# Kernel optimization log

Hardware: AMD Instinct MI355X
Metric: run time of the kernel (lower is better)

## Reference

```python
import jax, jax.numpy as jnp
import numpy as np

B, H, W, C = 32, 56, 56, 128
WS, NH, DEPTH = 7, 4, 2
SHIFT = WS // 2
N = WS * WS
HID = 4 * C
CPB = 512


def _layernorm(x, g, b, eps=1e-5):
    m = x.mean(-1, keepdims=True)
    v = ((x - m) ** 2).mean(-1, keepdims=True)
    return (x - m) * jax.lax.rsqrt(v + eps) * g + b


def _window_partition(x):
    b, h, w, c = x.shape
    x = x.reshape(b, h // WS, WS, w // WS, WS, c)
    return x.transpose(0, 1, 3, 2, 4, 5).reshape(-1, N, c)


def _window_reverse(xw, h, w):
    c = xw.shape[-1]
    b = xw.shape[0] // ((h // WS) * (w // WS))
    x = xw.reshape(b, h // WS, w // WS, WS, WS, c)
    return x.transpose(0, 1, 3, 2, 4, 5).reshape(b, h, w, c)


def _rel_index():
    coords = np.stack(np.meshgrid(np.arange(WS), np.arange(WS), indexing='ij'))
    flat = coords.reshape(2, -1)
    rel = (flat[:, :, None] - flat[:, None, :]).transpose(1, 2, 0).astype(np.int64)
    rel[..., 0] += WS - 1
    rel[..., 1] += WS - 1
    rel[..., 0] *= 2 * WS - 1
    return jnp.asarray(rel.sum(-1))  # [N, N]


def _coords_table():
    # SwinV2 log-spaced continuous relative coords table (pretrained_window_size=0 path)
    r = np.arange(-(WS - 1), WS, dtype=np.float32)
    t = np.stack(np.meshgrid(r, r, indexing='ij'), axis=-1)  # [2W-1, 2W-1, 2]
    t = t / (WS - 1) * 8.0
    t = np.sign(t) * np.log2(np.abs(t) + 1.0) / np.log2(8.0)
    return jnp.asarray(t.reshape(-1, 2))  # [(2W-1)^2, 2]


def _shift_mask():
    img = np.zeros((H, W), np.float32)
    cnt = 0
    for hs in (slice(0, -WS), slice(-WS, -SHIFT), slice(-SHIFT, None)):
        for ws_ in (slice(0, -WS), slice(-WS, -SHIFT), slice(-SHIFT, None)):
            img[hs, ws_] = cnt
            cnt += 1
    mw = np.asarray(_window_partition(jnp.asarray(img)[None, :, :, None])).reshape(-1, N)
    diff = mw[:, None, :] - mw[:, :, None]
    return jnp.asarray(np.where(diff != 0, -100.0, 0.0).astype(np.float32))  # [nW, N, N]


def _forward(x, qkv_w, q_bias, v_bias, logit_scale, cpb_w1, cpb_b1, cpb_w2,
             proj_w, proj_b, norm1_g, norm1_b, mlp_w1, mlp_b1, mlp_w2, mlp_b2,
             norm2_g, norm2_b, pm_g, pm_b, pm_w):
    rel_idx = _rel_index()
    table = _coords_table()
    smask = _shift_mask()
    for i in range(DEPTH):
        shift = 0 if i % 2 == 0 else SHIFT
        xs = jnp.roll(x, (-shift, -shift), axis=(1, 2)) if shift else x
        xw = _window_partition(xs)  # [B*nW, N, C]
        bias = jnp.concatenate([q_bias[i], jnp.zeros_like(q_bias[i]), v_bias[i]])
        qkv = (xw @ qkv_w[i] + bias).reshape(-1, N, 3, NH, C // NH).transpose(2, 0, 3, 1, 4)
        q, k, v = qkv[0], qkv[1], qkv[2]  # [B*nW, NH, N, hd]
        qn = q / jnp.maximum(jnp.linalg.norm(q, axis=-1, keepdims=True), 1e-12)
        kn = k / jnp.maximum(jnp.linalg.norm(k, axis=-1, keepdims=True), 1e-12)
        scale = jnp.exp(jnp.minimum(logit_scale[i], jnp.log(100.0)))  # [NH,1,1]
        attn = jnp.einsum('bhnd,bhmd->bhnm', qn, kn) * scale
        rpb = 16.0 * jax.nn.sigmoid(
            (jax.nn.relu(table @ cpb_w1[i] + cpb_b1[i]) @ cpb_w2[i])[rel_idx])  # [N,N,NH]
        attn = attn + rpb.transpose(2, 0, 1)[None]
        if shift:
            nW = smask.shape[0]
            attn = (attn.reshape(-1, nW, NH, N, N) + smask[None, :, None]).reshape(-1, NH, N, N)
        attn = jax.nn.softmax(attn, axis=-1)
        out = jnp.einsum('bhnm,bhmd->bnhd', attn, v).reshape(-1, N, C)
        out = out @ proj_w[i] + proj_b[i]
        xs = _window_reverse(out, H, W)
        if shift:
            xs = jnp.roll(xs, (shift, shift), axis=(1, 2))
        # SwinV2 post-norm residuals
        x = x + _layernorm(xs, norm1_g[i], norm1_b[i])
        y = jax.nn.gelu(x @ mlp_w1[i] + mlp_b1[i], approximate=False) @ mlp_w2[i] + mlp_b2[i]
        x = x + _layernorm(y, norm2_g[i], norm2_b[i])
    # PatchMerging: [B,H,W,C] -> [B,H/2,W/2,4C] -> norm -> Linear(4C,2C)
    xm = x.reshape(B, H // 2, 2, W // 2, 2, C).transpose(0, 1, 3, 2, 4, 5)
    xm = xm.reshape(B, H // 2, W // 2, 4 * C)
    return _layernorm(xm, pm_g, pm_b) @ pm_w


def setup_inputs() -> dict:
    key = jax.random.key(0)
    ks = jax.random.split(key, 8)
    s = 0.02
    rn = lambda k, shp: jax.random.normal(k, shp, jnp.float32) * s
    return dict(
        x=jax.random.normal(ks[0], (B, H, W, C), jnp.float32),
        qkv_w=rn(ks[1], (DEPTH, C, 3 * C)),
        q_bias=jnp.zeros((DEPTH, C), jnp.float32),
        v_bias=jnp.zeros((DEPTH, C), jnp.float32),
        logit_scale=jnp.full((DEPTH, NH, 1, 1), np.log(10.0), jnp.float32),
        cpb_w1=rn(ks[2], (DEPTH, 2, CPB)),
        cpb_b1=jnp.zeros((DEPTH, CPB), jnp.float32),
        cpb_w2=rn(ks[3], (DEPTH, CPB, NH)),
        proj_w=rn(ks[4], (DEPTH, C, C)),
        proj_b=jnp.zeros((DEPTH, C), jnp.float32),
        norm1_g=jnp.ones((DEPTH, C), jnp.float32),
        norm1_b=jnp.zeros((DEPTH, C), jnp.float32),
        mlp_w1=rn(ks[5], (DEPTH, C, HID)),
        mlp_b1=jnp.zeros((DEPTH, HID), jnp.float32),
        mlp_w2=rn(ks[6], (DEPTH, HID, C)),
        mlp_b2=jnp.zeros((DEPTH, C), jnp.float32),
        norm2_g=jnp.ones((DEPTH, C), jnp.float32),
        norm2_b=jnp.zeros((DEPTH, C), jnp.float32),
        pm_g=jnp.ones((4 * C,), jnp.float32),
        pm_b=jnp.zeros((4 * C,), jnp.float32),
        pm_w=rn(ks[7], (4 * C, 2 * C)),
    )


def reference(x, qkv_w, q_bias, v_bias, logit_scale, cpb_w1, cpb_b1, cpb_w2,
              proj_w, proj_b, norm1_g, norm1_b, mlp_w1, mlp_b1, mlp_w2, mlp_b2,
              norm2_g, norm2_b, pm_g, pm_b, pm_w):
    return _forward(x, qkv_w, q_bias, v_bias, logit_scale, cpb_w1, cpb_b1, cpb_w2,
                    proj_w, proj_b, norm1_g, norm1_b, mlp_w1, mlp_b1, mlp_w2, mlp_b2,
                    norm2_g, norm2_b, pm_g, pm_b, pm_w)
```

## Files before the change

### kernel.cpp

```cpp
#include <hip/hip_runtime.h>
#include <math.h>


namespace {
constexpr int kTok = 32 * 56 * 56;
}

typedef __attribute__((ext_vector_type(8))) short bf16x8;
typedef __attribute__((ext_vector_type(4))) float f32x4;

union FragU {
    int4 i4;
    bf16x8 b8;
    unsigned short u[8];
};

__device__ __forceinline__ short f2bf(float f) {
    unsigned u = __float_as_uint(f);
    return (short)((u + 0x7FFFu + ((u >> 16) & 1u)) >> 16);
}
__device__ __forceinline__ float bf2f(unsigned short u) {
    return __uint_as_float(((unsigned)u) << 16);
}
__device__ __forceinline__ unsigned cvt_pk_bf16(float a, float b) {
    unsigned r;
    asm("v_cvt_pk_bf16_f32 %0, %1, %2" : "=v"(r) : "v"(a), "v"(b));
    return r;
}
__device__ __forceinline__ float gelu_t(float x) {
    float x2 = x * x;
    float t0 = fmaf(0.044715f * x2, x, x);
    float e = exp2f(2.3022227f * t0);
    float r = __builtin_amdgcn_rcpf(e + 1.0f);
    return fmaf(-x, r, x);
}

__global__ __launch_bounds__(256) void k_cpb(
    const float* __restrict__ w1, const float* __restrict__ b1,
    const float* __restrict__ w2, float* __restrict__ out169) {
    int L = blockIdx.x / 169;
    int t = blockIdx.x % 169;
    const float* w1L = w1 + L * 1024;
    const float* b1L = b1 + L * 512;
    const float* w2L = w2 + L * 2048;
    float* outL = out169 + L * 704;
    int ia = t / 13, ib = t % 13;
    float r0 = (float)(ia - 6) * (8.0f / 6.0f);
    float s0 = (r0 > 0.f) ? 1.f : (r0 < 0.f ? -1.f : 0.f);
    float t0 = s0 * log2f(fabsf(r0) + 1.0f) * (1.0f / 3.0f);
    float r1 = (float)(ib - 6) * (8.0f / 6.0f);
    float s1 = (r1 > 0.f) ? 1.f : (r1 < 0.f ? -1.f : 0.f);
    float t1 = s1 * log2f(fabsf(r1) + 1.0f) * (1.0f / 3.0f);

    int tid = threadIdx.x;
    float p0 = 0, p1 = 0, p2 = 0, p3 = 0;
    for (int c = tid; c < 512; c += 256) {
        float hv = fmaxf(t0 * w1L[c] + t1 * w1L[512 + c] + b1L[c], 0.0f);
        p0 += hv * w2L[c * 4 + 0];
        p1 += hv * w2L[c * 4 + 1];
        p2 += hv * w2L[c * 4 + 2];
        p3 += hv * w2L[c * 4 + 3];
    }
    __shared__ float red[256][4];
    red[tid][0] = p0; red[tid][1] = p1; red[tid][2] = p2; red[tid][3] = p3;
    __syncthreads();
    for (int s = 128; s > 0; s >>= 1) {
        if (tid < s) {
            red[tid][0] += red[tid + s][0];
            red[tid][1] += red[tid + s][1];
            red[tid][2] += red[tid + s][2];
            red[tid][3] += red[tid + s][3];
        }
        __syncthreads();
    }
    if (tid < 4) outL[t * 4 + tid] = red[0][tid];
}

__global__ void k_rpb(const float* __restrict__ out169, float* __restrict__ rpb64) {
    int e2 = blockIdx.x * 256 + threadIdx.x;
    int L = e2 >> 14, e = e2 & 16383;
    int h = e >> 12, r = e & 4095;
    int i = r >> 6, j = r & 63;
    float val;
    if (j >= 49) {
        val = -30000.0f;
    } else if (i >= 49) {
        val = 0.0f;
    } else {
        int dp = i / 7 - j / 7 + 6;
        int dq = i % 7 - j % 7 + 6;
        float v = out169[L * 704 + (dp * 13 + dq) * 4 + h];
        val = 16.0f / (1.0f + expf(-v));
    }
    rpb64[e2] = val;
}

__device__ __forceinline__ void cvt_slot(
    const float* __restrict__ W, short* __restrict__ Wb, int slt, int Kb, int N) {
    int nn = slt & 63;
    int tmp = slt >> 6;
    int kb = tmp % Kb;
    int nt = tmp / Kb;
    int n = nt * 64 + nn;
    int k0 = kb * 8;
    union { int4 i4; short s8[8]; } u;
#pragma unroll
    for (int e = 0; e < 8; ++e) u.s8[e] = f2bf(W[(size_t)(k0 + e) * N + n]);
    int nns = (nn & ~3) | ((nn ^ kb) & 3);
    *(int4*)(Wb + (((size_t)tmp) * 64 + nns) * 8) = u.i4;
}

__global__ __launch_bounds__(256) void k_cvtall(
    const float* __restrict__ qkv_w, const float* __restrict__ proj_w,
    const float* __restrict__ mw1, const float* __restrict__ mw2,
    const float* __restrict__ pmw, short* __restrict__ wall) {
    int s = blockIdx.x * 256 + threadIdx.x;
    short* wqkvb  = wall;
    short* wprojb = wall + 98304;
    short* wm1b   = wall + 131072;
    short* wm2b   = wall + 262144;
    short* wpmb   = wall + 393216;
    if (s < 12288) {
        int L = s / 6144, r = s % 6144;
        cvt_slot(qkv_w + L * 49152, wqkvb + L * 49152, r, 16, 384);
    } else if (s < 16384) {
        int s2 = s - 12288;
        int L = s2 / 2048, r = s2 % 2048;
        cvt_slot(proj_w + L * 16384, wprojb + L * 16384, r, 16, 128);
    } else if (s < 32768) {
        int s2 = s - 16384;
        int L = s2 / 8192, r = s2 % 8192;
        cvt_slot(mw1 + L * 65536, wm1b + L * 65536, r, 16, 512);
    } else if (s < 49152) {
        int s2 = s - 32768;
        int L = s2 / 8192, r = s2 % 8192;
        cvt_slot(mw2 + L * 65536, wm2b + L * 65536, r, 64, 128);
    } else {
        cvt_slot(pmw, wpmb, s - 49152, 64, 256);
    }
}

__global__ __launch_bounds__(256) void k_cvtx(
    const float* __restrict__ x, short* __restrict__ xb) {
    size_t e = ((size_t)blockIdx.x * 256 + threadIdx.x) * 8;
    const float* src = x + e;
    float4 f0 = *(const float4*)src;
    float4 f1 = *(const float4*)(src + 4);
    union { int4 i4; short s8[8]; } u;
    u.s8[0] = f2bf(f0.x); u.s8[1] = f2bf(f0.y);
    u.s8[2] = f2bf(f0.z); u.s8[3] = f2bf(f0.w);
    u.s8[4] = f2bf(f1.x); u.s8[5] = f2bf(f1.y);
    u.s8[6] = f2bf(f1.z); u.s8[7] = f2bf(f1.w);
    *(int4*)(xb + e) = u.i4;
}

template <int K, int EPI, int NT>
__global__ __launch_bounds__(256) void k_gemm(
    const short* __restrict__ Ain, const short* __restrict__ Wb,
    const float* __restrict__ bias0, const float* __restrict__ bias1,
    void* __restrict__ Out, int ostride, int shift) {
    constexpr int Kb = K / 8;
    constexpr int NC = K / 128;
    __shared__ int4 As4[2048];
    __shared__ int4 Ws4[1024];
    int tid = threadIdx.x;
    int nwg = gridDim.x;
    int chunk = nwg >> 3;
    int lid = (blockIdx.x & 7) * chunk + (blockIdx.x >> 3);
    int mt = lid / NT, nt = lid - mt * NT;
    int mb = mt * 128;
    int w = tid >> 6, l = tid & 63, lr = l & 15, lg = l >> 4;
    const f32x4 fz = {0.f, 0.f, 0.f, 0.f};
    f32x4 acc[2][4];
#pragma unroll
    for (int mi = 0; mi < 2; ++mi)
#pragma unroll
        for (int ni = 0; ni < 4; ++ni) acc[mi][ni] = fz;

    for (int c = 0; c < NC; ++c) {
        if (c) __syncthreads();
#pragma unroll
        for (int it = 0; it < 8; ++it) {
            int s = it * 256 + tid;
            int m = s >> 4, kb = s & 15;
            int gm = mb + m;
            if (EPI == 1 && shift) {
                int b = gm / 3136, r = gm % 3136;
                int hh = r / 56 + shift; if (hh >= 56) hh -= 56;
                int ww = r % 56 + shift; if (ww >= 56) ww -= 56;
                gm = b * 3136 + hh * 56 + ww;
            }
            int slot = kb * 128 + ((m & ~7) | ((m ^ kb) & 7));
            As4[slot] = *(const int4*)(Ain + (size_t)gm * K + c * 128 + kb * 8);
        }
        {
            const int4* wsrc = (const int4*)(Wb + ((size_t)nt * Kb + c * 16) * 64 * 8);
#pragma unroll
            for (int it = 0; it < 4; ++it) Ws4[it * 256 + tid] = wsrc[it * 256 + tid];
        }
        __syncthreads();
#pragma unroll
        for (int kk = 0; kk < 4; ++kk) {
            int kbl = kk * 4 + lg;
            int m0 = w * 32 + lr;
            bf16x8 a0 = *(const bf16x8*)&As4[kbl * 128 + ((m0 & ~7) | ((m0 ^ kbl) & 7))];
            int m1 = m0 + 16;
            bf16x8 a1 = *(const bf16x8*)&As4[kbl * 128 + ((m1 & ~7) | ((m1 ^ kbl) & 7))];
#pragma unroll
            for (int ni = 0; ni < 4; ++ni) {
                int nn = lr + 16 * ni;
                bf16x8 bfr = *(const bf16x8*)&Ws4[kbl * 64 + ((nn & ~3) | ((nn ^ kbl) & 3))];
                acc[0][ni] = __builtin_amdgcn_mfma_f32_16x16x32_bf16(a0, bfr, acc[0][ni], 0, 0, 0);
                acc[1][ni] = __builtin_amdgcn_mfma_f32_16x16x32_bf16(a1, bfr, acc[1][ni], 0, 0, 0);
            }
        }
    }
#pragma unroll
    for (int ni = 0; ni < 4; ++ni) {
        int col = nt * 64 + ni * 16 + lr;
        float bv = 0.f;
        if (EPI == 1) bv = (col < 128) ? bias0[col] : ((col < 256) ? 0.f : bias1[col - 256]);
#pragma unroll
        for (int mi = 0; mi < 2; ++mi) {
#pragma unroll
            for (int r = 0; r < 4; ++r) {
                int row = mb + w * 32 + mi * 16 + lg * 4 + r;
                float v = acc[mi][ni][r] + bv;
                if (EPI == 0) {
                    ((float*)Out)[(size_t)row * ostride + col] = v;
                } else {
                    ((short*)Out)[(size_t)row * 384 + col] = f2bf(v);
                }
            }
        }
    }
}

template <int K, bool RF32>
__global__ __launch_bounds__(256) void k_gemm_ln(
    const short* __restrict__ Ain, const short* __restrict__ Wb,
    const float* __restrict__ bias, const float* __restrict__ g,
    const float* __restrict__ bt, const void* __restrict__ resid,
    short* __restrict__ xoutb, int shift) {
    constexpr int Kb = K / 8;
    constexpr int NC = K / 128;
    __shared__ int4 As4[1024];
    __shared__ int4 Ws4[2048];
    int tid = threadIdx.x;
    int mb = blockIdx.x * 64;
    int w = tid >> 6, l = tid & 63, lr = l & 15, lg = l >> 4;
    const f32x4 fz = {0.f, 0.f, 0.f, 0.f};
    f32x4 acc[8];
#pragma unroll
    for (int ni = 0; ni < 8; ++ni) acc[ni] = fz;

    for (int c = 0; c < NC; ++c) {
        if (c) __syncthreads();
#pragma unroll
        for (int it = 0; it < 4; ++it) {
            int s = it * 256 + tid;
            int m = s >> 4, kb = s & 15;
            int slot = kb * 64 + ((m & ~7) | ((m ^ kb) & 7));
            As4[slot] = *(const int4*)(Ain + (size_t)(mb + m) * K + c * 128 + kb * 8);
        }
        {
            const int4* w0 = (const int4*)(Wb + ((size_t)(c * 16)) * 64 * 8);
            const int4* w1 = (const int4*)(Wb + ((size_t)(Kb + c * 16)) * 64 * 8);
#pragma unroll
            for (int it = 0; it < 4; ++it) {
                Ws4[it * 256 + tid] = w0[it * 256 + tid];
                Ws4[1024 + it * 256 + tid] = w1[it * 256 + tid];
            }
        }
        __syncthreads();
#pragma unroll
        for (int kk = 0; kk < 4; ++kk) {
            int kbl = kk * 4 + lg;
            int m0 = w * 16 + lr;
            bf16x8 a0 = *(const bf16x8*)&As4[kbl * 64 + ((m0 & ~7) | ((m0 ^ kbl) & 7))];
#pragma unroll
            for (int ni = 0; ni < 8; ++ni) {
                int nn = lr + 16 * (ni & 3);
                bf16x8 bfr = *(const bf16x8*)&Ws4[(ni >> 2) * 1024 + kbl * 64 +
                                                  ((nn & ~3) | ((nn ^ kbl) & 3))];
                acc[ni] = __builtin_amdgcn_mfma_f32_16x16x32_bf16(a0, bfr, acc[ni], 0, 0, 0);
            }
        }
    }
    float bv[8], gv[8], btv[8];
#pragma unroll
    for (int ni = 0; ni < 8; ++ni) {
        int col = ni * 16 + lr;
        bv[ni] = bias[col]; gv[ni] = g[col]; btv[ni] = bt[col];
    }
#pragma unroll
    for (int r = 0; r < 4; ++r) {
        int row = mb + w * 16 + lg * 4 + r;
        float v[8];
        float s1 = 0.f, s2 = 0.f;
#pragma unroll
        for (int ni = 0; ni < 8; ++ni) {
            v[ni] = acc[ni][r] + bv[ni];
            s1 += v[ni];
            s2 = fmaf(v[ni], v[ni], s2);
        }
#pragma unroll
        for (int off = 8; off >= 1; off >>= 1) {
            s1 += __shfl_xor(s1, off);
            s2 += __shfl_xor(s2, off);
        }
        float mean = s1 * (1.0f / 128.0f);
        float var = s2 * (1.0f / 128.0f) - mean * mean;
        float rstd = rsqrtf(var + 1e-5f);
        int mo = row;
        if (shift) {
            int b = row / 3136, rr = row % 3136;
            int hh = rr / 56 + shift; if (hh >= 56) hh -= 56;
            int ww = rr % 56 + shift; if (ww >= 56) ww -= 56;
            mo = b * 3136 + hh * 56 + ww;
        }
        size_t base = (size_t)mo * 128;
#pragma unroll
        for (int ni = 0; ni < 8; ++ni) {
            int col = ni * 16 + lr;
            float rv = RF32 ? ((const float*)resid)[base + col]
                            : bf2f(((const unsigned short*)resid)[base + col]);
            float o = rv + (v[ni] - mean) * rstd * gv[ni] + btv[ni];
            xoutb[base + col] = f2bf(o);
        }
    }
}

__global__ __launch_bounds__(256) void k_mlp(
    short* __restrict__ xb, const short* __restrict__ W1b,
    const short* __restrict__ W2b, const float* __restrict__ b1,
    const float* __restrict__ b2, const float* __restrict__ g,
    const float* __restrict__ bt) {
    __shared__ int4 W1s[1024];
    __shared__ int4 W2s[1024];
    __shared__ short Hs[4 * 2304];
    int tid = threadIdx.x;
    int mb = blockIdx.x * 128;
    int w = tid >> 6, l = tid & 63, lr = l & 15, lg = l >> 4;
    const f32x4 fz = {0.f, 0.f, 0.f, 0.f};
    short* Hw = Hs + w * 2304;

    int4 xfrag[2][4];
#pragma unroll
    for (int mi = 0; mi < 2; ++mi)
#pragma unroll
        for (int kk = 0; kk < 4; ++kk)
            xfrag[mi][kk] = *(const int4*)(
                xb + (size_t)(mb + w * 32 + mi * 16 + lr) * 128 + kk * 32 + lg * 8);

    f32x4 acc2[2][8];
#pragma unroll
    for (int mi = 0; mi < 2; ++mi)
#pragma unroll
        for (int ni = 0; ni < 8; ++ni) acc2[mi][ni] = fz;

    int4 wr0, wr1, wr2, wr3, wr4, wr5, wr6, wr7;
#define LOADW(c)                                                            \
    {                                                                       \
        const int4* w1src = (const int4*)(W1b + (size_t)(c) * 8192);        \
        wr0 = w1src[tid]; wr1 = w1src[256 + tid];                           \
        wr2 = w1src[512 + tid]; wr3 = w1src[768 + tid];                     \
        const int4* w2a = (const int4*)(W2b + (size_t)((c) * 8) * 512);     \
        const int4* w2c = (const int4*)(W2b + (size_t)(64 + (c) * 8) * 512);\
        wr4 = w2a[tid]; wr5 = w2a[256 + tid];                               \
        wr6 = w2c[tid]; wr7 = w2c[256 + tid];                               \
    }
#define STOREW()                                                            \
    {                                                                       \
        W1s[tid] = wr0; W1s[256 + tid] = wr1;                               \
        W1s[512 + tid] = wr2; W1s[768 + tid] = wr3;                         \
        W2s[tid] = wr4; W2s[256 + tid] = wr5;                               \
        W2s[512 + tid] = wr6; W2s[768 + tid] = wr7;                         \
    }

    LOADW(0);
    STOREW();
    __syncthreads();

    for (int c = 0; c < 8; ++c) {
        if (c < 7) LOADW(c + 1);
        f32x4 a1[2][4];
#pragma unroll
        for (int mi = 0; mi < 2; ++mi)
#pragma unroll
            for (int ct = 0; ct < 4; ++ct) a1[mi][ct] = fz;
        __builtin_amdgcn_s_setprio(1);
#pragma unroll
        for (int kk = 0; kk < 4; ++kk) {
            int kbl = kk * 4 + lg;
            FragU xa0; xa0.i4 = xfrag[0][kk];
            FragU xa1; xa1.i4 = xfrag[1][kk];
#pragma unroll
            for (int ct = 0; ct < 4; ++ct) {
                int nn = lr + 16 * ct;
                bf16x8 w1f = *(const bf16x8*)&W1s[kbl * 64 + ((nn & ~3) | ((nn ^ kbl) & 3))];
                a1[0][ct] = __builtin_amdgcn_mfma_f32_16x16x32_bf16(w1f, xa0.b8, a1[0][ct], 0, 0, 0);
                a1[1][ct] = __builtin_amdgcn_mfma_f32_16x16x32_bf16(w1f, xa1.b8, a1[1][ct], 0, 0, 0);
            }
        }
        __builtin_amdgcn_s_setprio(0);
#pragma unroll
        for (int mi = 0; mi < 2; ++mi) {
#pragma unroll
            for (int ct = 0; ct < 4; ++ct) {
                float4 bb = *(const float4*)(b1 + c * 64 + ct * 16 + lg * 4);
                float h0 = gelu_t(a1[mi][ct][0] + bb.x);
                float h1 = gelu_t(a1[mi][ct][1] + bb.y);
                float h2 = gelu_t(a1[mi][ct][2] + bb.z);
                float h3 = gelu_t(a1[mi][ct][3] + bb.w);
                unsigned p0 = cvt_pk_bf16(h0, h1);
                unsigned p1 = cvt_pk_bf16(h2, h3);
                *(int2*)&Hw[(mi * 16 + lr) * 72 + ct * 16 + lg * 4] =
                    make_int2((int)p0, (int)p1);
            }
        }
        __builtin_amdgcn_s_setprio(1);
#pragma unroll
        for (int kc = 0; kc < 2; ++kc) {
            int kbl = kc * 4 + lg;
            FragU ha0; ha0.i4 = *(const int4*)&Hw[lr * 72 + kc * 32 + lg * 8];
            FragU ha1; ha1.i4 = *(const int4*)&Hw[(16 + lr) * 72 + kc * 32 + lg * 8];
#pragma unroll
            for (int ni = 0; ni < 8; ++ni) {
                int nn = lr + 16 * (ni & 3);
                bf16x8 w2f = *(const bf16x8*)&W2s[(ni >> 2) * 512 + kbl * 64 +
                                                  ((nn & ~3) | ((nn ^ kbl) & 3))];
                acc2[0][ni] = __builtin_amdgcn_mfma_f32_16x16x32_bf16(ha0.b8, w2f, acc2[0][ni], 0, 0, 0);
                acc2[1][ni] = __builtin_amdgcn_mfma_f32_16x16x32_bf16(ha1.b8, w2f, acc2[1][ni], 0, 0, 0);
            }
        }
        __builtin_amdgcn_s_setprio(0);
        if (c < 7) {
            __syncthreads();
            STOREW();
            __syncthreads();
        }
    }
#undef LOADW
#undef STOREW

    float bv[8], gv[8], btv[8];
#pragma unroll
    for (int ni = 0; ni < 8; ++ni) {
        int col = ni * 16 + lr;
        bv[ni] = b2[col]; gv[ni] = g[col]; btv[ni] = bt[col];
    }
#pragma unroll
    for (int mi = 0; mi < 2; ++mi) {
#pragma unroll
        for (int r = 0; r < 4; ++r) {
            int row = mb + w * 32 + mi * 16 + lg * 4 + r;
            float v[8];
            float s1 = 0.f, s2 = 0.f;
#pragma unroll
            for (int ni = 0; ni < 8; ++ni) {
                v[ni] = acc2[mi][ni][r] + bv[ni];
                s1 += v[ni];
                s2 = fmaf(v[ni], v[ni], s2);
            }
#pragma unroll
            for (int off = 8; off >= 1; off >>= 1) {
                s1 += __shfl_xor(s1, off);
                s2 += __shfl_xor(s2, off);
            }
            float mean = s1 * (1.0f / 128.0f);
            float var = s2 * (1.0f / 128.0f) - mean * mean;
            float rstd = rsqrtf(var + 1e-5f);
            size_t base = (size_t)row * 128;
#pragma unroll
            for (int ni = 0; ni < 8; ++ni) {
                int col = ni * 16 + lr;
                float rv = bf2f(((const unsigned short*)xb)[base + col]);
                float o = rv + (v[ni] - mean) * rstd * gv[ni] + btv[ni];
                xb[base + col] = f2bf(o);
            }
        }
    }
}

__global__ __launch_bounds__(256) void k_attn(
    const short* __restrict__ qkv, const float* __restrict__ rpb64,
    const float* __restrict__ ls, short* __restrict__ aout, int shift) {
    __shared__ short lds[4 * 3584];
    int wid = blockIdx.x;
    int b = wid >> 6, wrem = wid & 63;
    int wh = wrem >> 3, ww_ = wrem & 7;
    int h = threadIdx.x >> 6;
    int l = threadIdx.x & 63, lr = l & 15, lg = l >> 4;
    short* Pt = lds + h * 3584;
    short* Vt = Pt + 1152;
    float* invks = (float*)(Vt + 2304);
    int tokbase = b * 3136 + wh * 7 * 56 + ww_ * 7;

    float scale = __expf(fminf(ls[h], 4.6051702f));
    int4 qf[4], kf[4], vf[4];
    const int4 zero4 = make_int4(0, 0, 0, 0);
#pragma unroll
    for (int t = 0; t < 4; ++t) {
        int i = t * 16 + lr;
        bool valid = (i < 49);
        int tok = tokbase + (i / 7) * 56 + (i % 7);
        const short* base = qkv + (size_t)tok * 384 + h * 32 + lg * 8;
        qf[t] = valid ? *(const int4*)base : zero4;
        kf[t] = valid ? *(const int4*)(base + 128) : zero4;
    }
#pragma unroll
    for (int t = 0; t < 4; ++t) {
        int e = t * 64 + l;
        int j = e >> 2, dq = e & 3;
        if (j < 49) {
            int tok = tokbase + (j / 7) * 56 + (j % 7);
            vf[t] = *(const int4*)(qkv + (size_t)tok * 384 + 256 + h * 32 + dq * 8);
        } else {
            vf[t] = zero4;
        }
    }

    float invq[4];
#pragma unroll
    for (int t = 0; t < 4; ++t) {
        {
            FragU u; u.i4 = qf[t];
            float ss = 0.f;
#pragma unroll
            for (int e = 0; e < 8; ++e) { float x = bf2f(u.u[e]); ss = fmaf(x, x, ss); }
            ss += __shfl_xor(ss, 16);
            ss += __shfl_xor(ss, 32);
            invq[t] = scale / fmaxf(sqrtf(ss), 1e-12f);
        }
        {
            FragU u; u.i4 = kf[t];
            float ss = 0.f;
#pragma unroll
            for (int e = 0; e < 8; ++e) { float x = bf2f(u.u[e]); ss = fmaf(x, x, ss); }
            ss += __shfl_xor(ss, 16);
            ss += __shfl_xor(ss, 32);
            float ik = 1.0f / fmaxf(sqrtf(ss), 1e-12f);
            if (l < 16) invks[t * 16 + l] = ik;
        }
    }

    for (int t = l; t < 480; t += 64) {
        Vt[(t / 15) * 72 + 49 + (t % 15)] = 0;
    }
#pragma unroll
    for (int t = 0; t < 4; ++t) {
        int e = t * 64 + l;
        int j = e >> 2, dq = e & 3;
        if (j < 49) {
            FragU u; u.i4 = vf[t];
#pragma unroll
            for (int ee = 0; ee < 8; ++ee) Vt[(dq * 8 + ee) * 72 + j] = (short)u.u[ee];
        }
    }

    float ika[4][4];
#pragma unroll
    for (int jt = 0; jt < 4; ++jt) {
        float4 v4 = *(const float4*)&invks[jt * 16 + lg * 4];
        ika[jt][0] = v4.x; ika[jt][1] = v4.y; ika[jt][2] = v4.z; ika[jt][3] = v4.w;
    }

    bool edge = (shift != 0) && ((wh == 7) || (ww_ == 7));
    const float* rbase = rpb64 + h * 4096;
    const f32x4 fz = {0.f, 0.f, 0.f, 0.f};
    f32x4 oacc[2][4];
#pragma unroll
    for (int mi = 0; mi < 2; ++mi)
#pragma unroll
        for (int ni = 0; ni < 4; ++ni) oacc[mi][ni] = fz;

#pragma unroll
    for (int qt = 0; qt < 4; ++qt) {
        f32x4 at[4];
        __builtin_amdgcn_s_setprio(1);
#pragma unroll
        for (int jt = 0; jt < 4; ++jt) {
            FragU a; a.i4 = kf[jt];
            FragU bq; bq.i4 = qf[qt];
            at[jt] = __builtin_amdgcn_mfma_f32_16x16x32_bf16(a.b8, bq.b8, fz, 0, 0, 0);
        }
        __builtin_amdgcn_s_setprio(0);

        float iq = invq[qt];
        int qi = qt * 16 + lr;
        int qc = (qi < 49) ? qi : 48;
        int rlq = 0, clq = 0;
        if (edge) {
            rlq = (wh == 7) ? ((qc / 7) < 4 ? 1 : 2) : 0;
            clq = (ww_ == 7) ? ((qc % 7) < 4 ? 1 : 2) : 0;
        }
#pragma unroll
        for (int jt = 0; jt < 4; ++jt) {
            float4 rv = *(const float4*)(rbase + qc * 64 + jt * 16 + lg * 4);
            float rr[4] = {rv.x, rv.y, rv.z, rv.w};
#pragma unroll
            for (int r = 0; r < 4; ++r) {
                float v = fmaf(at[jt][r] * ika[jt][r], iq, rr[r]);
                if (edge) {
                    int j = jt * 16 + lg * 4 + r;
                    int jc = (j < 49) ? j : 48;
                    int rlk = (wh == 7) ? ((jc / 7) < 4 ? 1 : 2) : 0;
                    int clk = (ww_ == 7) ? ((jc % 7) < 4 ? 1 : 2) : 0;
                    if (rlk != rlq || clk != clq) v -= 100.0f;
                }
                at[jt][r] = v;
            }
        }
        float m = -1e30f;
#pragma unroll
        for (int jt = 0; jt < 4; ++jt)
#pragma unroll
            for (int r = 0; r < 4; ++r) m = fmaxf(m, at[jt][r]);
        m = fmaxf(m, __shfl_xor(m, 16));
        m = fmaxf(m, __shfl_xor(m, 32));
        float s = 0.f;
#pragma unroll
        for (int jt = 0; jt < 4; ++jt)
#pragma unroll
            for (int r = 0; r < 4; ++r) {
                float p = __expf(at[jt][r] - m);
                at[jt][r] = p;
                s += p;
            }
        s += __shfl_xor(s, 16);
        s += __shfl_xor(s, 32);
        float inv = 1.0f / s;
#pragma unroll
        for (int jt = 0; jt < 4; ++jt) {
            unsigned lo = cvt_pk_bf16(at[jt][0] * inv, at[jt][1] * inv);
            unsigned hi = cvt_pk_bf16(at[jt][2] * inv, at[jt][3] * inv);
            *(int2*)&Pt[lr * 72 + jt * 16 + lg * 4] = make_int2((int)lo, (int)hi);
        }
        __builtin_amdgcn_s_setprio(1);
#pragma unroll
        for (int kc = 0; kc < 2; ++kc) {
            FragU pb;
            pb.i4 = *(const int4*)&Pt[lr * 72 + kc * 32 + lg * 8];
#pragma unroll
            for (int mi = 0; mi < 2; ++mi) {
                FragU va;
                va.i4 = *(const int4*)&Vt[(mi * 16 + lr) * 72 + kc * 32 + lg * 8];
                oacc[mi][qt] = __builtin_amdgcn_mfma_f32_16x16x32_bf16(
                    va.b8, pb.b8, oacc[mi][qt], 0, 0, 0);
            }
        }
        __builtin_amdgcn_s_setprio(0);
    }

#pragma unroll
    for (int ni = 0; ni < 4; ++ni) {
        int qrow = ni * 16 + lr;
        if (qrow < 49) {
            int tok = tokbase + (qrow / 7) * 56 + (qrow % 7);
#pragma unroll
            for (int mi = 0; mi < 2; ++mi) {
                unsigned lo = cvt_pk_bf16(oacc[mi][ni][0], oacc[mi][ni][1]);
                unsigned hi = cvt_pk_bf16(oacc[mi][ni][2], oacc[mi][ni][3]);
                *(int2*)&aout[(size_t)tok * 128 + h * 32 + mi * 16 + lg * 4] =
                    make_int2((int)lo, (int)hi);
            }
        }
    }
}

__global__ __launch_bounds__(256) void k_pmln(
    const short* __restrict__ x, const float* __restrict__ g,
    const float* __restrict__ bt, short* __restrict__ outb) {
    int m2 = blockIdx.x * 4 + (threadIdx.x >> 6);
    int l = threadIdx.x & 63;
    int b = m2 / 784, r = m2 % 784;
    int h2 = r / 28, w2 = r % 28;
    int q0 = l * 8;
    int i2 = q0 >> 8, j2 = (q0 >> 7) & 1, c = q0 & 127;
    const short* src = x + (size_t)((b * 56 + 2 * h2 + i2) * 56 + 2 * w2 + j2) * 128 + c;
    FragU u; u.i4 = *(const int4*)src;
    float v[8];
#pragma unroll
    for (int e = 0; e < 8; ++e) v[e] = bf2f(u.u[e]);
    float s1 = 0.f, s2 = 0.f;
#pragma unroll
    for (int e = 0; e < 8; ++e) { s1 += v[e]; s2 = fmaf(v[e], v[e], s2); }
#pragma unroll
    for (int off = 32; off >= 1; off >>= 1) {
        s1 += __shfl_xor(s1, off);
        s2 += __shfl_xor(s2, off);
    }
    float mean = s1 * (1.0f / 512.0f);
    float var = s2 * (1.0f / 512.0f) - mean * mean;
    float rstd = rsqrtf(var + 1e-5f);
    union { int4 i4; short s8[8]; } o;
#pragma unroll
    for (int e = 0; e < 8; ++e)
        o.s8[e] = f2bf((v[e] - mean) * rstd * g[q0 + e] + bt[q0 + e]);
    *(int4*)(outb + (size_t)m2 * 512 + q0) = o.i4;
}

extern "C" void kernel_launch(void* const* d_in, const int* in_sizes, int n_in,
                              void* d_out, int out_size, void* d_ws, size_t ws_size,
                              hipStream_t stream) {
    const float* x_in   = (const float*)d_in[0];
    const float* qkv_w  = (const float*)d_in[1];
    const float* q_bias = (const float*)d_in[2];
    const float* v_bias = (const float*)d_in[3];
    const float* lscale = (const float*)d_in[4];
    const float* cpb_w1 = (const float*)d_in[5];
    const float* cpb_b1 = (const float*)d_in[6];
    const float* cpb_w2 = (const float*)d_in[7];
    const float* proj_w = (const float*)d_in[8];
    const float* proj_b = (const float*)d_in[9];
    const float* n1g    = (const float*)d_in[10];
    const float* n1b    = (const float*)d_in[11];
    const float* mw1    = (const float*)d_in[12];
    const float* mb1    = (const float*)d_in[13];
    const float* mw2    = (const float*)d_in[14];
    const float* mb2    = (const float*)d_in[15];
    const float* n2g    = (const float*)d_in[16];
    const float* n2b    = (const float*)d_in[17];
    const float* pmg    = (const float*)d_in[18];
    const float* pmb    = (const float*)d_in[19];
    const float* pmw    = (const float*)d_in[20];
    float* out = (float*)d_out;

    float* wsf    = (float*)d_ws;
    short* wall   = (short*)wsf;
    short* wqkvb  = wall;
    short* wprojb = wall + 98304;
    short* wm1b   = wall + 131072;
    short* wm2b   = wall + 262144;
    short* wpmb   = wall + 393216;
    float* out169 = wsf + 262144;
    float* rpb64  = out169 + 1408;

    float* R1      = wsf + (size_t)12845056;
    short* qkvb    = (short*)R1;
    short* attnout = (short*)(R1 + (size_t)19267584);
    short* pmin    = (short*)R1;
    short* xb      = (short*)(R1 + (size_t)25690112);

    k_cvtall<<<256, 256, 0, stream>>>(qkv_w, proj_w, mw1, mw2, pmw, wall);
    k_cpb<<<338, 256, 0, stream>>>(cpb_w1, cpb_b1, cpb_w2, out169);
    k_rpb<<<128, 256, 0, stream>>>(out169, rpb64);
    k_cvtx<<<6272, 256, 0, stream>>>(x_in, xb);

    for (int i = 0; i < 2; ++i) {
        int shift = i ? 3 : 0;
        k_gemm<128, 1, 6><<<4704, 256, 0, stream>>>(
            xb, wqkvb + i * 49152, q_bias + i * 128, v_bias + i * 128,
            qkvb, 384, shift);
        k_attn<<<2048, 256, 0, stream>>>(
            qkvb, rpb64 + i * 16384, lscale + i * 4, attnout, shift);
        if (i == 0) {
            k_gemm_ln<128, true><<<1568, 256, 0, stream>>>(
                attnout, wprojb, proj_b, n1g, n1b, x_in, xb, shift);
        } else {
            k_gemm_ln<128, false><<<1568, 256, 0, stream>>>(
                attnout, wprojb + 16384, proj_b + 128, n1g + 128, n1b + 128,
                xb, xb, shift);
        }
        k_mlp<<<784, 256, 0, stream>>>(
            xb, wm1b + i * 65536, wm2b + i * 65536, mb1 + i * 512,
            mb2 + i * 128, n2g + i * 128, n2b + i * 128);
    }
    k_pmln<<<6272, 256, 0, stream>>>(xb, pmg, pmb, pmin);
    k_gemm<512, 0, 4><<<784, 256, 0, stream>>>(
        pmin, wpmb, nullptr, nullptr, out, 256, 0);
}
```

Before: 380.4 us.

## Fuse QKV projection into window attention kernel and drop MLP weight prefetch

The separate QKV GEMM kernel is removed. Each attention workgroup now computes its window's 49x384 QKV tile with MFMA straight from the bf16 activations, handling the shift, and stages it in LDS. This avoids writing and re-reading the full QKV tensor through global memory and removes one launch per layer, at the cost of more LDS per block and each block re-reading the QKV weights. The MLP kernel's register-prefetch double buffering of weights is also replaced by plain synchronous loads into LDS, which may expose load latency.

Result: faster. 354.8 us (-6.7%).

```diff
diff --git a/kernel.cpp b/kernel.cpp
--- a/kernel.cpp
+++ b/kernel.cpp
@@ -113,7 +113,9 @@
 __global__ __launch_bounds__(256) void k_cvtall(
     const float* __restrict__ qkv_w, const float* __restrict__ proj_w,
     const float* __restrict__ mw1, const float* __restrict__ mw2,
-    const float* __restrict__ pmw, short* __restrict__ wall) {
+    const float* __restrict__ pmw, const float* __restrict__ qb,
+    const float* __restrict__ vb, short* __restrict__ wall,
+    float* __restrict__ bias384) {
     int s = blockIdx.x * 256 + threadIdx.x;
     short* wqkvb  = wall;
     short* wprojb = wall + 98304;
@@ -135,8 +137,14 @@
         int s2 = s - 32768;
         int L = s2 / 8192, r = s2 % 8192;
         cvt_slot(mw2 + L * 65536, wm2b + L * 65536, r, 64, 128);
-    } else {
+    } else if (s < 65536) {
         cvt_slot(pmw, wpmb, s - 49152, 64, 256);
+    } else if (s < 66304) {
+        int t = s - 65536;
+        int L = t / 384, f = t % 384;
+        float v = (f < 128) ? qb[L * 128 + f]
+                            : ((f < 256) ? 0.0f : vb[L * 128 + f - 256]);
+        bias384[t] = v;
     }
 }
 
@@ -154,11 +162,10 @@
     *(int4*)(xb + e) = u.i4;
 }
 
-template <int K, int EPI, int NT>
+template <int K, int NT>
 __global__ __launch_bounds__(256) void k_gemm(
     const short* __restrict__ Ain, const short* __restrict__ Wb,
-    const float* __restrict__ bias0, const float* __restrict__ bias1,
-    void* __restrict__ Out, int ostride, int shift) {
+    float* __restrict__ Out, int ostride) {
     constexpr int Kb = K / 8;
     constexpr int NC = K / 128;
     __shared__ int4 As4[2048];
@@ -183,15 +190,8 @@
         for (int it = 0; it < 8; ++it) {
             int s = it * 256 + tid;
             int m = s >> 4, kb = s & 15;
-            int gm = mb + m;
-            if (EPI == 1 && shift) {
-                int b = gm / 3136, r = gm % 3136;
-                int hh = r / 56 + shift; if (hh >= 56) hh -= 56;
-                int ww = r % 56 + shift; if (ww >= 56) ww -= 56;
-                gm = b * 3136 + hh * 56 + ww;
-            }
             int slot = kb * 128 + ((m & ~7) | ((m ^ kb) & 7));
-            As4[slot] = *(const int4*)(Ain + (size_t)gm * K + c * 128 + kb * 8);
+            As4[slot] = *(const int4*)(Ain + (size_t)(mb + m) * K + c * 128 + kb * 8);
         }
         {
             const int4* wsrc = (const int4*)(Wb + ((size_t)nt * Kb + c * 16) * 64 * 8);
@@ -218,19 +218,12 @@
 #pragma unroll
     for (int ni = 0; ni < 4; ++ni) {
         int col = nt * 64 + ni * 16 + lr;
-        float bv = 0.f;
-        if (EPI == 1) bv = (col < 128) ? bias0[col] : ((col < 256) ? 0.f : bias1[col - 256]);
 #pragma unroll
         for (int mi = 0; mi < 2; ++mi) {
 #pragma unroll
             for (int r = 0; r < 4; ++r) {
                 int row = mb + w * 32 + mi * 16 + lg * 4 + r;
-                float v = acc[mi][ni][r] + bv;
-                if (EPI == 0) {
-                    ((float*)Out)[(size_t)row * ostride + col] = v;
-                } else {
-                    ((short*)Out)[(size_t)row * 384 + col] = f2bf(v);
-                }
+                Out[(size_t)row * ostride + col] = acc[mi][ni][r];
             }
         }
     }
@@ -359,31 +352,21 @@
 #pragma unroll
         for (int ni = 0; ni < 8; ++ni) acc2[mi][ni] = fz;
 
-    int4 wr0, wr1, wr2, wr3, wr4, wr5, wr6, wr7;
-#define LOADW(c)                                                            \
-    {                                                                       \
-        const int4* w1src = (const int4*)(W1b + (size_t)(c) * 8192);        \
-        wr0 = w1src[tid]; wr1 = w1src[256 + tid];                           \
-        wr2 = w1src[512 + tid]; wr3 = w1src[768 + tid];                     \
-        const int4* w2a = (const int4*)(W2b + (size_t)((c) * 8) * 512);     \
-        const int4* w2c = (const int4*)(W2b + (size_t)(64 + (c) * 8) * 512);\
-        wr4 = w2a[tid]; wr5 = w2a[256 + tid];                               \
-        wr6 = w2c[tid]; wr7 = w2c[256 + tid];                               \
-    }
-#define STOREW()                                                            \
-    {                                                                       \
-        W1s[tid] = wr0; W1s[256 + tid] = wr1;                               \
-        W1s[512 + tid] = wr2; W1s[768 + tid] = wr3;                         \
-        W2s[tid] = wr4; W2s[256 + tid] = wr5;                               \
-        W2s[512 + tid] = wr6; W2s[768 + tid] = wr7;                         \
-    }
-
-    LOADW(0);
-    STOREW();
-    __syncthreads();
-
     for (int c = 0; c < 8; ++c) {
-        if (c < 7) LOADW(c + 1);
+        __syncthreads();
+        {
+            const int4* w1src = (const int4*)(W1b + (size_t)c * 8192);
+#pragma unroll
+            for (int it = 0; it < 4; ++it) W1s[it * 256 + tid] = w1src[it * 256 + tid];
+            const int4* w2a = (const int4*)(W2b + (size_t)(c * 8) * 512);
+            const int4* w2c = (const int4*)(W2b + (size_t)(64 + c * 8) * 512);
+#pragma unroll
+            for (int it = 0; it < 2; ++it) {
+                W2s[it * 256 + tid] = w2a[it * 256 + tid];
+                W2s[512 + it * 256 + tid] = w2c[it * 256 + tid];
+            }
+        }
+        __syncthreads();
         f32x4 a1[2][4];
 #pragma unroll
         for (int mi = 0; mi < 2; ++mi)
@@ -435,14 +418,7 @@
             }
         }
         __builtin_amdgcn_s_setprio(0);
-        if (c < 7) {
-            __syncthreads();
-            STOREW();
-            __syncthreads();
-        }
-    }
-#undef LOADW
-#undef STOREW
+    }
 
     float bv[8], gv[8], btv[8];
 #pragma unroll
@@ -484,41 +460,74 @@
 }
 
 __global__ __launch_bounds__(256) void k_attn(
-    const short* __restrict__ qkv, const float* __restrict__ rpb64,
+    const short* __restrict__ xb, const short* __restrict__ Wq,
+    const float* __restrict__ bias384, const float* __restrict__ rpb64,
     const float* __restrict__ ls, short* __restrict__ aout, int shift) {
-    __shared__ short lds[4 * 3584];
+    __shared__ short qkvs[64 * 392];
+    __shared__ short pvt[4 * 3584];
     int wid = blockIdx.x;
     int b = wid >> 6, wrem = wid & 63;
     int wh = wrem >> 3, ww_ = wrem & 7;
-    int h = threadIdx.x >> 6;
-    int l = threadIdx.x & 63, lr = l & 15, lg = l >> 4;
-    short* Pt = lds + h * 3584;
+    int tid = threadIdx.x;
+    int w = tid >> 6;
+    int l = tid & 63, lr = l & 15, lg = l >> 4;
+    int tokbase = b * 3136 + wh * 7 * 56 + ww_ * 7;
+    const f32x4 fz = {0.f, 0.f, 0.f, 0.f};
+
+    {
+        int ti = w * 16 + lr;
+        bool valid = (ti < 49);
+        int4 xfrag[4];
+        const int4 zero4 = make_int4(0, 0, 0, 0);
+        if (valid) {
+            int m = tokbase + (ti / 7) * 56 + (ti % 7);
+            if (shift) {
+                int bb2 = m / 3136, rr = m % 3136;
+                int hh = rr / 56 + shift; if (hh >= 56) hh -= 56;
+                int ww2 = rr % 56 + shift; if (ww2 >= 56) ww2 -= 56;
+                m = bb2 * 3136 + hh * 56 + ww2;
+            }
+#pragma unroll
+            for (int kk = 0; kk < 4; ++kk)
+                xfrag[kk] = *(const int4*)(xb + (size_t)m * 128 + kk * 32 + lg * 8);
+        } else {
+#pragma unroll
+            for (int kk = 0; kk < 4; ++kk) xfrag[kk] = zero4;
+        }
+        short* orow = qkvs + (w * 16 + lr) * 392;
+#pragma unroll
+        for (int ft = 0; ft < 24; ++ft) {
+            f32x4 a = fz;
+            int n = ft * 16 + lr;
+            int nt = n >> 6, nn = n & 63;
+#pragma unroll
+            for (int kk = 0; kk < 4; ++kk) {
+                int kbl = kk * 4 + lg;
+                int nns = (nn & ~3) | ((nn ^ kbl) & 3);
+                bf16x8 wf = *(const bf16x8*)(Wq + (((size_t)nt * 16 + kbl) * 64 + nns) * 8);
+                FragU xa; xa.i4 = xfrag[kk];
+                a = __builtin_amdgcn_mfma_f32_16x16x32_bf16(wf, xa.b8, a, 0, 0, 0);
+            }
+            float4 bb = *(const float4*)(bias384 + ft * 16 + lg * 4);
+            unsigned p0 = cvt_pk_bf16(a[0] + bb.x, a[1] + bb.y);
+            unsigned p1 = cvt_pk_bf16(a[2] + bb.z, a[3] + bb.w);
+            *(int2*)&orow[ft * 16 + lg * 4] = make_int2((int)p0, (int)p1);
+        }
+    }
+    __syncthreads();
+
+    int h = w;
+    short* Pt = pvt + h * 3584;
     short* Vt = Pt + 1152;
     float* invks = (float*)(Vt + 2304);
-    int tokbase = b * 3136 + wh * 7 * 56 + ww_ * 7;
 
     float scale = __expf(fminf(ls[h], 4.6051702f));
-    int4 qf[4], kf[4], vf[4];
-    const int4 zero4 = make_int4(0, 0, 0, 0);
+    int4 qf[4], kf[4];
 #pragma unroll
     for (int t = 0; t < 4; ++t) {
-        int i = t * 16 + lr;
-        bool valid = (i < 49);
-        int tok = tokbase + (i / 7) * 56 + (i % 7);
-        const short* base = qkv + (size_t)tok * 384 + h * 32 + lg * 8;
-        qf[t] = valid ? *(const int4*)base : zero4;
-        kf[t] = valid ? *(const int4*)(base + 128) : zero4;
-    }
-#pragma unroll
-    for (int t = 0; t < 4; ++t) {
-        int e = t * 64 + l;
-        int j = e >> 2, dq = e & 3;
-        if (j < 49) {
-            int tok = tokbase + (j / 7) * 56 + (j % 7);
-            vf[t] = *(const int4*)(qkv + (size_t)tok * 384 + 256 + h * 32 + dq * 8);
-        } else {
-            vf[t] = zero4;
-        }
+        const short* base = qkvs + (t * 16 + lr) * 392 + h * 32 + lg * 8;
+        qf[t] = *(const int4*)base;
+        kf[t] = *(const int4*)(base + 128);
     }
 
     float invq[4];
@@ -553,7 +562,8 @@
         int e = t * 64 + l;
         int j = e >> 2, dq = e & 3;
         if (j < 49) {
-            FragU u; u.i4 = vf[t];
+            FragU u;
+            u.i4 = *(const int4*)(qkvs + j * 392 + 256 + h * 32 + dq * 8);
 #pragma unroll
             for (int ee = 0; ee < 8; ++ee) Vt[(dq * 8 + ee) * 72 + j] = (short)u.u[ee];
         }
@@ -568,7 +578,6 @@
 
     bool edge = (shift != 0) && ((wh == 7) || (ww_ == 7));
     const float* rbase = rpb64 + h * 4096;
-    const f32x4 fz = {0.f, 0.f, 0.f, 0.f};
     f32x4 oacc[2][4];
 #pragma unroll
     for (int mi = 0; mi < 2; ++mi)
@@ -736,25 +745,24 @@
     short* wpmb   = wall + 393216;
     float* out169 = wsf + 262144;
     float* rpb64  = out169 + 1408;
+    float* bias384 = rpb64 + 32768;
 
     float* R1      = wsf + (size_t)12845056;
-    short* qkvb    = (short*)R1;
     short* attnout = (short*)(R1 + (size_t)19267584);
     short* pmin    = (short*)R1;
     short* xb      = (short*)(R1 + (size_t)25690112);
 
-    k_cvtall<<<256, 256, 0, stream>>>(qkv_w, proj_w, mw1, mw2, pmw, wall);
+    k_cvtall<<<260, 256, 0, stream>>>(qkv_w, proj_w, mw1, mw2, pmw,
+                                      q_bias, v_bias, wall, bias384);
     k_cpb<<<338, 256, 0, stream>>>(cpb_w1, cpb_b1, cpb_w2, out169);
     k_rpb<<<128, 256, 0, stream>>>(out169, rpb64);
     k_cvtx<<<6272, 256, 0, stream>>>(x_in, xb);
 
     for (int i = 0; i < 2; ++i) {
         int shift = i ? 3 : 0;
-        k_gemm<128, 1, 6><<<4704, 256, 0, stream>>>(
-            xb, wqkvb + i * 49152, q_bias + i * 128, v_bias + i * 128,
-            qkvb, 384, shift);
         k_attn<<<2048, 256, 0, stream>>>(
-            qkvb, rpb64 + i * 16384, lscale + i * 4, attnout, shift);
+            xb, wqkvb + i * 49152, bias384 + i * 384, rpb64 + i * 16384,
+            lscale + i * 4, attnout, shift);
         if (i == 0) {
             k_gemm_ln<128, true><<<1568, 256, 0, stream>>>(
                 attnout, wprojb, proj_b, n1g, n1b, x_in, xb, shift);
@@ -768,6 +776,5 @@
             mb2 + i * 128, n2g + i * 128, n2b + i * 128);
     }
     k_pmln<<<6272, 256, 0, stream>>>(xb, pmg, pmb, pmin);
-    k_gemm<512, 0, 4><<<784, 256, 0, stream>>>(
-        pmin, wpmb, nullptr, nullptr, out, 256, 0);
-}
+    k_gemm<512, 4><<<784, 256, 0, stream>>>(pmin, wpmb, out, 256);
+}
```
